# Kernel tuning notes

Hardware: AMD Instinct MI355X
Metric: run time of the kernel (lower is better)

## Reference

```python
import jax, jax.numpy as jnp
import numpy as np

NEG_SLOPE = 0.2  # PyG GATConv default negative_slope
EPS = 1e-16


def gat_conv(x, src, dst, num_nodes, W, a_src, a_dst, bias, heads, out_c, concat):
    """PyG-style GATConv (eval mode, self-loops already appended).
    x: [N, F_in]; src/dst: [E] (edge j->i with src=j, dst=i).
    W: [F_in, heads*out_c]; a_src/a_dst: [heads, out_c]; bias: [heads*out_c] or [out_c].
    """
    xw = (x @ W).reshape(num_nodes, heads, out_c)          # [N, H, C]
    alpha_src = jnp.sum(xw * a_src, axis=-1)               # [N, H]
    alpha_dst = jnp.sum(xw * a_dst, axis=-1)               # [N, H]
    e = jax.nn.leaky_relu(alpha_src[src] + alpha_dst[dst], NEG_SLOPE)  # [E, H]
    # numerically stable segment softmax over edges grouped by destination node
    m = jax.ops.segment_max(e, dst, num_segments=num_nodes)            # [N, H]
    e = jnp.exp(e - m[dst])
    denom = jax.ops.segment_sum(e, dst, num_segments=num_nodes)        # [N, H]
    alpha = e / (denom[dst] + EPS)                                     # [E, H]
    # weighted scatter-sum aggregation of source messages
    out = jax.ops.segment_sum(xw[src] * alpha[:, :, None], dst, num_segments=num_nodes)  # [N, H, C]
    if concat:
        out = out.reshape(num_nodes, heads * out_c)
    else:
        out = out.mean(axis=1)
    return out + bias


def setup_inputs() -> dict:
    key = jax.random.key(0)
    ks = jax.random.split(key, 12)
    N, E = 50000, 800000
    F_in, Hid, H1, Out = 512, 32, 8, 64

    def xavier(k, shape, gain=1.414):
        fan_in, fan_out = shape[0], shape[-1] if len(shape) == 2 else int(np.prod(shape[1:]))
        a = gain * np.sqrt(6.0 / (fan_in + fan_out))
        return jax.random.uniform(k, shape, jnp.float32, -a, a)

    x = jax.random.normal(ks[0], (N, F_in), jnp.float32)
    edge_index = jax.random.randint(ks[1], (2, E), 0, N, jnp.int64)

    W1 = xavier(ks[2], (F_in, H1 * Hid))
    a_src1 = xavier(ks[3], (H1, Hid))
    a_dst1 = xavier(ks[4], (H1, Hid))
    b1 = jnp.zeros((H1 * Hid,), jnp.float32)

    W2 = xavier(ks[5], (H1 * Hid, Out))
    a_src2 = xavier(ks[6], (1, Out))
    a_dst2 = xavier(ks[7], (1, Out))
    b2 = jnp.zeros((Out,), jnp.float32)

    return {"x": x, "edge_index": edge_index,
            "W1": W1, "a_src1": a_src1, "a_dst1": a_dst1, "b1": b1,
            "W2": W2, "a_src2": a_src2, "a_dst2": a_dst2, "b2": b2}


def reference(x, edge_index, W1, a_src1, a_dst1, b1, W2, a_src2, a_dst2, b2):
    N = x.shape[0]
    # add self-loops (PyG GATConv default add_self_loops=True)
    loop = jnp.arange(N, dtype=edge_index.dtype)
    src = jnp.concatenate([edge_index[0], loop])
    dst = jnp.concatenate([edge_index[1], loop])

    # eval mode: all dropouts are identity
    h = gat_conv(x, src, dst, N, W1, a_src1, a_dst1, b1, heads=8, out_c=32, concat=True)
    h = jax.nn.elu(h)
    h = gat_conv(h, src, dst, N, W2, a_src2, a_dst2, b2, heads=1, out_c=64, concat=False)
    return jax.nn.log_softmax(h, axis=1)
```

## Files before the change

### kernel.cpp

```cpp
#include <hip/hip_runtime.h>
#include <hip/hip_bf16.h>


typedef __attribute__((ext_vector_type(8)))  __bf16          bf16x8;
typedef __attribute__((ext_vector_type(8)))  unsigned short  ushort8;
typedef __attribute__((ext_vector_type(16))) float           f32x16;
typedef __attribute__((ext_vector_type(2)))  float           f32x2;

#define NEG_SLOPE 0.2f
#define EPS_GAT 1e-16f

static __device__ __forceinline__ float lrelu(float x) {
    return x > 0.0f ? x : NEG_SLOPE * x;
}
static __device__ __forceinline__ unsigned short f2bf(float f) {
    unsigned u = __float_as_uint(f);
    return (unsigned short)((u + 0x7fffu + ((u >> 16) & 1u)) >> 16);
}
static __device__ __forceinline__ float bf2f(unsigned short v) {
    return __uint_as_float(((unsigned)v) << 16);
}
static __device__ __forceinline__ unsigned encf(float x) {
    unsigned u = __float_as_uint(x);
    return (u >> 31) ? ~u : (u | 0x80000000u);
}
static __device__ __forceinline__ float decf(unsigned e) {
    unsigned u = (e >> 31) ? (e & 0x7fffffffu) : ~e;
    return __uint_as_float(u);
}

__global__ void k_hist_w(const void* __restrict__ eix, int* __restrict__ counts,
                         int E, int EB,
                         const float* __restrict__ W1, const float* __restrict__ W2,
                         unsigned short* __restrict__ w1t, unsigned short* __restrict__ w2t) {
    int b = blockIdx.x;
    if (b < EB) {
        int i = b * 256 + threadIdx.x;
        unsigned w = ((const unsigned*)eix)[2 * min(i, E - 1) + 1];
        bool is64 = (__syncthreads_or((int)(w != 0u)) == 0);
        if (i < E) {
            int d = is64 ? (int)((const long long*)eix)[E + i]
                         : ((const int*)eix)[E + i];
            atomicAdd(&counts[d], 1);
        }
    } else {
        int t = (b - EB) * 256 + threadIdx.x;
        if (t < 512 * 256) {
            int k = t >> 8, m = t & 255;
            w1t[m * 512 + k] = f2bf(W1[t]);
        } else {
            int u = t - 512 * 256;
            if (u < 256 * 64) {
                int k = u >> 6, m = u & 63;
                w2t[m * 256 + k] = f2bf(W2[u]);
            }
        }
    }
}

__global__ void k_scan1(const int* __restrict__ counts, int* __restrict__ rowp,
                        int* __restrict__ bsum, int N) {
    __shared__ int s[256];
    int t = threadIdx.x, i = blockIdx.x * 256 + t;
    int v = (i < N) ? counts[i] : 0;
    s[t] = v;
    __syncthreads();
    for (int off = 1; off < 256; off <<= 1) {
        int u = (t >= off) ? s[t - off] : 0;
        __syncthreads();
        s[t] += u;
        __syncthreads();
    }
    if (i < N) rowp[i] = s[t] - v;
    if (t == 255) bsum[blockIdx.x] = s[255];
}

__global__ void k_scan2(const int* __restrict__ bsum, int* __restrict__ boff,
                        int* __restrict__ rowp_last, int NB) {
    __shared__ int s[256];
    int t = threadIdx.x;
    int v = (t < NB) ? bsum[t] : 0;
    s[t] = v;
    __syncthreads();
    for (int off = 1; off < 256; off <<= 1) {
        int u = (t >= off) ? s[t - off] : 0;
        __syncthreads();
        s[t] += u;
        __syncthreads();
    }
    if (t < NB) boff[t] = s[t] - v;
    if (t == 255) *rowp_last = s[255];
}

__global__ void k_scan3(int* __restrict__ rowp, int* __restrict__ cursor,
                        const int* __restrict__ boff, int N) {
    int i = blockIdx.x * 256 + threadIdx.x;
    if (i < N) {
        int r = rowp[i] + boff[blockIdx.x];
        rowp[i] = r;
        cursor[i] = r;
    }
}

__global__ void k_fill(const void* __restrict__ eix, int* __restrict__ cursor,
                       int* __restrict__ ssrc, int E) {
    int i = blockIdx.x * 256 + threadIdx.x;
    unsigned w = ((const unsigned*)eix)[2 * min(i, E - 1) + 1];
    bool is64 = (__syncthreads_or((int)(w != 0u)) == 0);
    if (i >= E) return;
    int s, d;
    if (is64) {
        s = (int)((const long long*)eix)[i];
        d = (int)((const long long*)eix)[E + i];
    } else {
        s = ((const int*)eix)[i];
        d = ((const int*)eix)[E + i];
    }
    int pos = atomicAdd(&cursor[d], 1);
    ssrc[pos] = s;
}

template <int BM, int BN, int NT, bool AF32, bool OUTBF>
__global__ __launch_bounds__(NT) void k_gemm(const void* __restrict__ Ain,
                                             const unsigned short* __restrict__ Bt,
                                             void* __restrict__ Cout, int Nrows, int K) {
    constexpr int LD = 40;
    constexpr int AIT = BM * 4 / NT;
    constexpr int BIT = BN * 4 / NT;
    __shared__ __align__(16) unsigned short As[BM * LD];
    __shared__ __align__(16) unsigned short Bs[BN * LD];
    const int tid = threadIdx.x;
    const int blockRow = blockIdx.x * BM;
    const int wave = tid >> 6, lane = tid & 63;
    constexpr int WR = BM / 64;
    const int wr = wave % WR, wc = wave / WR;
    const int m = lane & 31;
    const int ksel = (lane >> 5) * 8;

    f32x16 acc00{}, acc01{}, acc10{}, acc11{};

    float4  af0[AIT], af1[AIT];
    ushort8 ab[AIT];
    ushort8 bb[BIT];

    auto loadA = [&](int kt) {
        #pragma unroll
        for (int i = 0; i < AIT; ++i) {
            int idx = tid + i * NT;
            int r = idx >> 2, kc = (idx & 3) * 8;
            int grow = blockRow + r;
            if constexpr (AF32) {
                const float* A = (const float*)Ain;
                if (grow < Nrows) {
                    const float* ap = A + (size_t)grow * K + kt + kc;
                    af0[i] = *(const float4*)ap;
                    af1[i] = *(const float4*)(ap + 4);
                } else {
                    af0[i] = make_float4(0.f, 0.f, 0.f, 0.f);
                    af1[i] = make_float4(0.f, 0.f, 0.f, 0.f);
                }
            } else {
                const unsigned short* A = (const unsigned short*)Ain;
                ushort8 o{};
                if (grow < Nrows) o = *(const ushort8*)(A + (size_t)grow * K + kt + kc);
                ab[i] = o;
            }
        }
    };
    auto loadB = [&](int kt) {
        #pragma unroll
        for (int i = 0; i < BIT; ++i) {
            int idx = tid + i * NT;
            int r = idx >> 2, kc = (idx & 3) * 8;
            bb[i] = *(const ushort8*)(Bt + (size_t)r * K + kt + kc);
        }
    };
    auto writeAB = [&]() {
        #pragma unroll
        for (int i = 0; i < AIT; ++i) {
            int idx = tid + i * NT;
            int r = idx >> 2, kc = (idx & 3) * 8;
            if constexpr (AF32) {
                union { ushort8 u; __hip_bfloat162 h[4]; } cv;
                cv.h[0] = __float22bfloat162_rn(make_float2(af0[i].x, af0[i].y));
                cv.h[1] = __float22bfloat162_rn(make_float2(af0[i].z, af0[i].w));
                cv.h[2] = __float22bfloat162_rn(make_float2(af1[i].x, af1[i].y));
                cv.h[3] = __float22bfloat162_rn(make_float2(af1[i].z, af1[i].w));
                *(ushort8*)&As[r * LD + kc] = cv.u;
            } else {
                *(ushort8*)&As[r * LD + kc] = ab[i];
            }
        }
        #pragma unroll
        for (int i = 0; i < BIT; ++i) {
            int idx = tid + i * NT;
            int r = idx >> 2, kc = (idx & 3) * 8;
            *(ushort8*)&Bs[r * LD + kc] = bb[i];
        }
    };

    loadA(0);
    loadB(0);
    for (int kt = 0; kt < K; kt += 32) {
        writeAB();
        __syncthreads();
        if (kt + 32 < K) {
            loadA(kt + 32);
            loadB(kt + 32);
        }
        #pragma unroll
        for (int kk = 0; kk < 32; kk += 16) {
            bf16x8 a0 = *(const bf16x8*)&As[(wr * 64 +      m) * LD + kk + ksel];
            bf16x8 a1 = *(const bf16x8*)&As[(wr * 64 + 32 + m) * LD + kk + ksel];
            bf16x8 b0 = *(const bf16x8*)&Bs[(wc * 64 +      m) * LD + kk + ksel];
            bf16x8 b1 = *(const bf16x8*)&Bs[(wc * 64 + 32 + m) * LD + kk + ksel];
            acc00 = __builtin_amdgcn_mfma_f32_32x32x16_bf16(a0, b0, acc00, 0, 0, 0);
            acc01 = __builtin_amdgcn_mfma_f32_32x32x16_bf16(a0, b1, acc01, 0, 0, 0);
            acc10 = __builtin_amdgcn_mfma_f32_32x32x16_bf16(a1, b0, acc10, 0, 0, 0);
            acc11 = __builtin_amdgcn_mfma_f32_32x32x16_bf16(a1, b1, acc11, 0, 0, 0);
        }
        __syncthreads();
    }

    const int dcol = wc * 64 + (lane & 31);
    const int dquad = 4 * (lane >> 5);
    auto store_tile = [&](const f32x16& a, int rt, int ct) {
        #pragma unroll
        for (int r = 0; r < 16; ++r) {
            int row = blockRow + wr * 64 + rt * 32 + (r & 3) + 8 * (r >> 2) + dquad;
            if (row < Nrows) {
                size_t off = (size_t)row * BN + dcol + ct * 32;
                if constexpr (OUTBF) ((unsigned short*)Cout)[off] = f2bf(a[r]);
                else                 ((float*)Cout)[off] = a[r];
            }
        }
    };
    store_tile(acc00, 0, 0); store_tile(acc01, 0, 1);
    store_tile(acc10, 1, 0); store_tile(acc11, 1, 1);
}

__global__ void k_alpha(const unsigned short* __restrict__ xw, const float* __restrict__ a_s,
                        const float* __restrict__ a_d, float* __restrict__ os,
                        float* __restrict__ od, unsigned* __restrict__ Menc,
                        int NH, int H, int C) {
    __shared__ float red[256];
    int t = blockIdx.x * 256 + threadIdx.x;
    float s = -1e30f, d = 0.f;
    if (t < NH) {
        int n = t / H, h = t - n * H;
        const unsigned short* row = xw + (size_t)n * H * C + h * C;
        s = 0.f;
        for (int c = 0; c < C; c += 8) {
            ushort8 v = *(const ushort8*)(row + c);
            #pragma unroll
            for (int q = 0; q < 8; ++q) {
                float f = bf2f(v[q]);
                s += f * a_s[h * C + c + q];
                d += f * a_d[h * C + c + q];
            }
        }
        os[t] = s; od[t] = d;
    }
    red[threadIdx.x] = s;
    __syncthreads();
    for (int off = 128; off >= H; off >>= 1) {
        if (threadIdx.x < off) red[threadIdx.x] = fmaxf(red[threadIdx.x], red[threadIdx.x + off]);
        __syncthreads();
    }
    if ((int)threadIdx.x < H) atomicMax(&Menc[threadIdx.x], encf(red[threadIdx.x]));
}

__global__ __launch_bounds__(256, 6) void k_agg_l1(
        const unsigned short* __restrict__ xw1, const float* __restrict__ asrc,
        const float* __restrict__ adst, const unsigned* __restrict__ Menc,
        const float* __restrict__ b1, const int* __restrict__ rp,
        const int* __restrict__ ssrc, unsigned short* __restrict__ hbf, int N) {
    int wid = (blockIdx.x * 256 + threadIdx.x) >> 6;
    if (wid >= N) return;
    const int lane = threadIdx.x & 63;
    const int g  = lane >> 4;
    const int q  = lane & 15;
    const int f0 = q * 16;
    const int h  = q >> 1;
    const int ih = wid * 8 + h;
    const float ad = adst[ih];
    const float m  = lrelu(decf(Menc[h]) + ad);
    f32x2 acc[8];
    float s;
    {
        float w = (g == 0) ? __expf(lrelu(asrc[ih] + ad) - m) : 0.0f;
        const unsigned short* pr = xw1 + (size_t)wid * 256 + f0;
        ushort8 lo = *(const ushort8*)pr;
        ushort8 hi = *(const ushort8*)(pr + 8);
        s = w;
        const unsigned* dl = (const unsigned*)&lo;
        const unsigned* dh = (const unsigned*)&hi;
        #pragma unroll
        for (int p = 0; p < 4; ++p) {
            acc[p].x     = w * __uint_as_float(dl[p] << 16);
            acc[p].y     = w * __uint_as_float(dl[p] & 0xffff0000u);
            acc[4 + p].x = w * __uint_as_float(dh[p] << 16);
            acc[4 + p].y = w * __uint_as_float(dh[p] & 0xffff0000u);
        }
    }
    const int e0 = rp[wid], e1 = rp[wid + 1];
    if (e0 < e1) {
        const int NQ = (e1 - e0 + 3) >> 2;

        auto LDJ = [&](int base, int& j, bool& v) {
            v = base + g < e1;
            j = ssrc[min(base + g, e1 - 1)];
        };
        auto LDD = [&](int j, float& as, ushort8& lo, ushort8& hi) {
            as = asrc[j * 8 + h];
            const unsigned short* p = xw1 + ((size_t)j << 8) + f0;
            lo = *(const ushort8*)p;
            hi = *(const ushort8*)(p + 8);
        };
        auto CONS = [&](bool v, float as, const ushort8& lo, const ushort8& hi) {
            float w = v ? __expf(lrelu(as + ad) - m) : 0.0f;
            s += w;
            f32x2 wp; wp.x = w; wp.y = w;
            const unsigned* dl = (const unsigned*)&lo;
            const unsigned* dh = (const unsigned*)&hi;
            #pragma unroll
            for (int p = 0; p < 4; ++p) {
                f32x2 x;
                x.x = __uint_as_float(dl[p] << 16);
                x.y = __uint_as_float(dl[p] & 0xffff0000u);
                asm("v_pk_fma_f32 %0, %1, %2, %3"
                    : "=v"(acc[p]) : "v"(x), "v"(wp), "v"(acc[p]));
            }
            #pragma unroll
            for (int p = 0; p < 4; ++p) {
                f32x2 x;
                x.x = __uint_as_float(dh[p] << 16);
                x.y = __uint_as_float(dh[p] & 0xffff0000u);
                asm("v_pk_fma_f32 %0, %1, %2, %3"
                    : "=v"(acc[4 + p]) : "v"(x), "v"(wp), "v"(acc[4 + p]));
            }
        };

        int j0, j1, j2, j3; bool v0, v1, v2, v3;
        float as0, as1; ushort8 lo0, hi0, lo1, hi1;
        LDJ(e0,      j0, v0);
        LDJ(e0 + 4,  j1, v1);
        LDD(j0, as0, lo0, hi0);
        LDJ(e0 + 8,  j2, v2);
        LDD(j1, as1, lo1, hi1);
        LDJ(e0 + 12, j3, v3);

        #pragma unroll 2
        for (int k = 0; k < NQ - 2; ++k) {
            int jN; bool vN;
            LDJ(e0 + 4 * k + 16, jN, vN);
            float as2; ushort8 lo2, hi2;
            LDD(j2, as2, lo2, hi2);
            CONS(v0, as0, lo0, hi0);
            v0 = v1; as0 = as1; lo0 = lo1; hi0 = hi1;
            v1 = v2; as1 = as2; lo1 = lo2; hi1 = hi2;
            v2 = v3; j2 = j3;
            v3 = vN; j3 = jN;
        }
        CONS(v0, as0, lo0, hi0);
        if (NQ >= 2) CONS(v1, as1, lo1, hi1);
    }
    s += __shfl_xor(s, 16, 64);
    s += __shfl_xor(s, 32, 64);
    #pragma unroll
    for (int p = 0; p < 8; ++p) {
        acc[p].x += __shfl_xor(acc[p].x, 16, 64);
        acc[p].x += __shfl_xor(acc[p].x, 32, 64);
        acc[p].y += __shfl_xor(acc[p].y, 16, 64);
        acc[p].y += __shfl_xor(acc[p].y, 32, 64);
    }
    float inv = 1.0f / (s + EPS_GAT);
    f32x2 p0 = (g & 2) ? ((g & 1) ? acc[6] : acc[4]) : ((g & 1) ? acc[2] : acc[0]);
    f32x2 p1 = (g & 2) ? ((g & 1) ? acc[7] : acc[5]) : ((g & 1) ? acc[3] : acc[1]);
    int fw = f0 + g * 4;
    float vv[4] = { p0.x, p0.y, p1.x, p1.y };
    ushort4 o;
    #pragma unroll
    for (int i = 0; i < 4; ++i) {
        float v = vv[i] * inv + b1[fw + i];
        v = v > 0.f ? v : expm1f(v);
        ((unsigned short*)&o)[i] = f2bf(v);
    }
    *(ushort4*)(hbf + (size_t)wid * 256 + fw) = o;
}

__global__ __launch_bounds__(256, 6) void k_agg_l2(
        const unsigned short* __restrict__ xw2, const float* __restrict__ asrc,
        const float* __restrict__ adst, const unsigned* __restrict__ Menc,
        const float* __restrict__ b2, const int* __restrict__ rp,
        const int* __restrict__ ssrc, float* __restrict__ out, int N) {
    int wid = (blockIdx.x * 256 + threadIdx.x) >> 6;
    if (wid >= N) return;
    const int lane = threadIdx.x & 63;
    const int g  = lane >> 3;
    const int q  = lane & 7;
    const int f0 = q * 8;
    const float ad = adst[wid];
    const float m = lrelu(decf(Menc[0]) + ad);
    f32x2 acc[4];
    float s;
    {
        float w = (g == 0) ? __expf(lrelu(asrc[wid] + ad) - m) : 0.0f;
        ushort8 xv = *(const ushort8*)(xw2 + (size_t)wid * 64 + f0);
        s = w;
        const unsigned* dx = (const unsigned*)&xv;
        #pragma unroll
        for (int p = 0; p < 4; ++p) {
            acc[p].x = w * __uint_as_float(dx[p] << 16);
            acc[p].y = w * __uint_as_float(dx[p] & 0xffff0000u);
        }
    }
    const int e0 = rp[wid], e1 = rp[wid + 1];
    if (e0 < e1) {
        const int NQ = (e1 - e0 + 7) >> 3;

        auto LDJ = [&](int base, int& j, bool& v) {
            v = base + g < e1;
            j = ssrc[min(base + g, e1 - 1)];
        };
        auto LDD = [&](int j, float& as, ushort8& xv) {
            as = asrc[j];
            xv = *(const ushort8*)(xw2 + ((size_t)j << 6) + f0);
        };
        auto CONS = [&](bool v, float as, const ushort8& xv) {
            float w = v ? __expf(lrelu(as + ad) - m) : 0.0f;
            s += w;
            f32x2 wp; wp.x = w; wp.y = w;
            const unsigned* dx = (const unsigned*)&xv;
            #pragma unroll
            for (int p = 0; p < 4; ++p) {
                f32x2 x;
                x.x = __uint_as_float(dx[p] << 16);
                x.y = __uint_as_float(dx[p] & 0xffff0000u);
                asm("v_pk_fma_f32 %0, %1, %2, %3"
                    : "=v"(acc[p]) : "v"(x), "v"(wp), "v"(acc[p]));
            }
        };

        int j0, j1, j2, j3; bool v0, v1, v2, v3;
        float as0, as1; ushort8 xv0, xv1;
        LDJ(e0,      j0, v0);
        LDJ(e0 + 8,  j1, v1);
        LDD(j0, as0, xv0);
        LDJ(e0 + 16, j2, v2);
        LDD(j1, as1, xv1);
        LDJ(e0 + 24, j3, v3);

        #pragma unroll 2
        for (int k = 0; k < NQ - 2; ++k) {
            int jN; bool vN;
            LDJ(e0 + 8 * k + 32, jN, vN);
            float as2; ushort8 xv2;
            LDD(j2, as2, xv2);
            CONS(v0, as0, xv0);
            v0 = v1; as0 = as1; xv0 = xv1;
            v1 = v2; as1 = as2; xv1 = xv2;
            v2 = v3; j2 = j3;
            v3 = vN; j3 = jN;
        }
        CONS(v0, as0, xv0);
        if (NQ >= 2) CONS(v1, as1, xv1);
    }
    s += __shfl_xor(s, 8, 64);
    s += __shfl_xor(s, 16, 64);
    s += __shfl_xor(s, 32, 64);
    #pragma unroll
    for (int p = 0; p < 4; ++p) {
        acc[p].x += __shfl_xor(acc[p].x, 8, 64);
        acc[p].x += __shfl_xor(acc[p].x, 16, 64);
        acc[p].x += __shfl_xor(acc[p].x, 32, 64);
        acc[p].y += __shfl_xor(acc[p].y, 8, 64);
        acc[p].y += __shfl_xor(acc[p].y, 16, 64);
        acc[p].y += __shfl_xor(acc[p].y, 32, 64);
    }
    float inv = 1.0f / (s + EPS_GAT);
    float val[8];
    float mx = -1e30f;
    #pragma unroll
    for (int i = 0; i < 8; ++i) {
        float a = (i & 1) ? acc[i >> 1].y : acc[i >> 1].x;
        val[i] = a * inv + b2[f0 + i];
        mx = fmaxf(mx, val[i]);
    }
    #pragma unroll
    for (int off = 4; off > 0; off >>= 1) mx = fmaxf(mx, __shfl_xor(mx, off, 64));
    float sm = 0.f;
    #pragma unroll
    for (int i = 0; i < 8; ++i) sm += __expf(val[i] - mx);
    #pragma unroll
    for (int off = 4; off > 0; off >>= 1) sm += __shfl_xor(sm, off, 64);
    float lse = mx + logf(sm);
    if (g == 0) {
        float4 o0 = make_float4(val[0] - lse, val[1] - lse, val[2] - lse, val[3] - lse);
        float4 o1 = make_float4(val[4] - lse, val[5] - lse, val[6] - lse, val[7] - lse);
        *(float4*)(out + (size_t)wid * 64 + f0)     = o0;
        *(float4*)(out + (size_t)wid * 64 + f0 + 4) = o1;
    }
}

static inline int cdiv(int a, int b) { return (a + b - 1) / b; }

extern "C" void kernel_launch(void* const* d_in, const int* in_sizes, int n_in,
                              void* d_out, int out_size, void* d_ws, size_t ws_size,
                              hipStream_t stream) {
    const float* x   = (const float*)d_in[0];
    const void*  eix = d_in[1];
    const float* W1  = (const float*)d_in[2];
    const float* as1 = (const float*)d_in[3];
    const float* ad1 = (const float*)d_in[4];
    const float* b1  = (const float*)d_in[5];
    const float* W2  = (const float*)d_in[6];
    const float* as2 = (const float*)d_in[7];
    const float* ad2 = (const float*)d_in[8];
    const float* b2  = (const float*)d_in[9];
    float* out = (float*)d_out;

    const int N = in_sizes[0] / 512;
    const int E = in_sizes[1] / 2;
    const int EB = cdiv(E, 256);
    const int WB = cdiv(512 * 256 + 256 * 64, 256);
    const int NB = cdiv(N, 256);
    const int NB1 = cdiv(N * 8, 256);
    const int NB2 = cdiv(N, 256);
    (void)n_in; (void)out_size; (void)ws_size;

    char* base = (char*)d_ws;
    size_t o = 0;
    auto alloc = [&](size_t bytes) -> char* {
        o = (o + 255) & ~(size_t)255;
        char* p = base + o;
        o += bytes;
        return p;
    };
    unsigned short* xw1b  = (unsigned short*)alloc((size_t)N * 256 * 2);
    unsigned short* hbf   = (unsigned short*)alloc((size_t)N * 256 * 2);
    unsigned short* xw2b  = (unsigned short*)alloc((size_t)N * 64 * 2);
    float*          asrc1 = (float*)alloc((size_t)N * 8 * 4);
    float*          adst1 = (float*)alloc((size_t)N * 8 * 4);
    float*          asrc2 = (float*)alloc((size_t)N * 4);
    float*          adst2 = (float*)alloc((size_t)N * 4);
    size_t zero_begin = (o + 255) & ~(size_t)255;
    unsigned*       Menc  = (unsigned*)alloc(16 * 4);
    int*            counts= (int*)alloc((size_t)N * 4);
    size_t zero_end = o;
    int*            cursor= (int*)alloc((size_t)N * 4);
    int*            rowp  = (int*)alloc((size_t)(N + 1) * 4);
    int*            bsum  = (int*)alloc(256 * 4);
    int*            boff  = (int*)alloc(256 * 4);
    unsigned short* w1t   = (unsigned short*)alloc(512 * 256 * 2);
    unsigned short* w2t   = (unsigned short*)alloc(256 * 64 * 2);
    int*            ssrc  = (int*)alloc((size_t)E * 4);

    hipMemsetAsync(base + zero_begin, 0, zero_end - zero_begin, stream);

    k_hist_w<<<EB + WB, 256, 0, stream>>>(eix, counts, E, EB, W1, W2, w1t, w2t);
    k_scan1<<<NB, 256, 0, stream>>>(counts, rowp, bsum, N);
    k_scan2<<<1, 256, 0, stream>>>(bsum, boff, rowp + N, NB);
    k_scan3<<<NB, 256, 0, stream>>>(rowp, cursor, boff, N);
    k_fill<<<EB, 256, 0, stream>>>(eix, cursor, ssrc, E);

    k_gemm<128, 256, 512, true, true><<<cdiv(N, 128), 512, 0, stream>>>(x, w1t, xw1b, N, 512);
    k_alpha<<<NB1, 256, 0, stream>>>(xw1b, as1, ad1, asrc1, adst1, Menc, N * 8, 8, 32);
    k_agg_l1<<<cdiv(N * 64, 256), 256, 0, stream>>>(xw1b, asrc1, adst1, Menc, b1,
                                                    rowp, ssrc, hbf, N);
    k_gemm<256, 64, 256, false, true><<<cdiv(N, 256), 256, 0, stream>>>(hbf, w2t, xw2b, N, 256);
    k_alpha<<<NB2, 256, 0, stream>>>(xw2b, as2, ad2, asrc2, adst2, Menc + 8, N, 1, 64);
    k_agg_l2<<<cdiv(N * 64, 256), 256, 0, stream>>>(xw2b, asrc2, adst2, Menc + 8, b2,
                                                    rowp, ssrc, out, N);
}
```

Measured before the change: 416.7 us.

## Store layer-1 features head-major and aggregate one head per block

The first GEMM now writes its output head-major ([H][N][32]), and the alpha kernel reads and writes in that layout. The layer-1 aggregation kernel is restructured so each block handles a single head for four nodes. Each wave processes 16 edges at a time, and each lane gathers a 16-byte slice of one head's row instead of full 512-byte rows. The aim is better cache locality, since each head's 3.2MB slice fits in cache when blocks are grouped by head, at the cost of more edge-index loads and a shallower prefetch pipeline than the previous four-stage software pipeline.

After: 582.0 us. +39.7%, slower.

```diff
diff --git a/kernel.cpp b/kernel.cpp
--- a/kernel.cpp
+++ b/kernel.cpp
@@ -120,7 +120,7 @@
     ssrc[pos] = s;
 }
 
-template <int BM, int BN, int NT, bool AF32, bool OUTBF>
+template <int BM, int BN, int NT, bool AF32, bool OUTBF, bool OUTHM>
 __global__ __launch_bounds__(NT) void k_gemm(const void* __restrict__ Ain,
                                              const unsigned short* __restrict__ Bt,
                                              void* __restrict__ Cout, int Nrows, int K) {
@@ -229,7 +229,12 @@
         for (int r = 0; r < 16; ++r) {
             int row = blockRow + wr * 64 + rt * 32 + (r & 3) + 8 * (r >> 2) + dquad;
             if (row < Nrows) {
-                size_t off = (size_t)row * BN + dcol + ct * 32;
+                int col = dcol + ct * 32;
+                size_t off;
+                if constexpr (OUTHM)
+                    off = ((size_t)(col >> 5) * Nrows + row) * 32 + (col & 31);
+                else
+                    off = (size_t)row * BN + col;
                 if constexpr (OUTBF) ((unsigned short*)Cout)[off] = f2bf(a[r]);
                 else                 ((float*)Cout)[off] = a[r];
             }
@@ -242,13 +247,13 @@
 __global__ void k_alpha(const unsigned short* __restrict__ xw, const float* __restrict__ a_s,
                         const float* __restrict__ a_d, float* __restrict__ os,
                         float* __restrict__ od, unsigned* __restrict__ Menc,
-                        int NH, int H, int C) {
+                        int NH, int H, int C, int Nn) {
     __shared__ float red[256];
     int t = blockIdx.x * 256 + threadIdx.x;
     float s = -1e30f, d = 0.f;
     if (t < NH) {
         int n = t / H, h = t - n * H;
-        const unsigned short* row = xw + (size_t)n * H * C + h * C;
+        const unsigned short* row = xw + ((size_t)h * Nn + n) * C;
         s = 0.f;
         for (int c = 0; c < C; c += 8) {
             ushort8 v = *(const ushort8*)(row + c);
@@ -259,7 +264,8 @@
                 d += f * a_d[h * C + c + q];
             }
         }
-        os[t] = s; od[t] = d;
+        size_t oi = (size_t)h * Nn + n;
+        os[oi] = s; od[oi] = d;
     }
     red[threadIdx.x] = s;
     __syncthreads();
@@ -271,122 +277,86 @@
 }
 
 __global__ __launch_bounds__(256, 6) void k_agg_l1(
-        const unsigned short* __restrict__ xw1, const float* __restrict__ asrc,
-        const float* __restrict__ adst, const unsigned* __restrict__ Menc,
+        const unsigned short* __restrict__ xwh,
+        const float* __restrict__ asrc,
+        const float* __restrict__ adst,
+        const unsigned* __restrict__ Menc,
         const float* __restrict__ b1, const int* __restrict__ rp,
         const int* __restrict__ ssrc, unsigned short* __restrict__ hbf, int N) {
-    int wid = (blockIdx.x * 256 + threadIdx.x) >> 6;
-    if (wid >= N) return;
+    const int h  = blockIdx.x & 7;
+    const int n  = (blockIdx.x >> 3) * 4 + (threadIdx.x >> 6);
+    if (n >= N) return;
     const int lane = threadIdx.x & 63;
-    const int g  = lane >> 4;
-    const int q  = lane & 15;
-    const int f0 = q * 16;
-    const int h  = q >> 1;
-    const int ih = wid * 8 + h;
-    const float ad = adst[ih];
+    const int g  = lane & 15;
+    const int c8 = (lane >> 4) * 8;
+    const size_t hN = (size_t)h * N;
+    const float ad = adst[hN + n];
     const float m  = lrelu(decf(Menc[h]) + ad);
-    f32x2 acc[8];
+    f32x2 acc[4];
     float s;
     {
-        float w = (g == 0) ? __expf(lrelu(asrc[ih] + ad) - m) : 0.0f;
-        const unsigned short* pr = xw1 + (size_t)wid * 256 + f0;
-        ushort8 lo = *(const ushort8*)pr;
-        ushort8 hi = *(const ushort8*)(pr + 8);
+        float w = (g == 0) ? __expf(lrelu(asrc[hN + n] + ad) - m) : 0.0f;
+        ushort8 xv = *(const ushort8*)(xwh + (hN + n) * 32 + c8);
         s = w;
-        const unsigned* dl = (const unsigned*)&lo;
-        const unsigned* dh = (const unsigned*)&hi;
+        const unsigned* dx = (const unsigned*)&xv;
         #pragma unroll
         for (int p = 0; p < 4; ++p) {
-            acc[p].x     = w * __uint_as_float(dl[p] << 16);
-            acc[p].y     = w * __uint_as_float(dl[p] & 0xffff0000u);
-            acc[4 + p].x = w * __uint_as_float(dh[p] << 16);
-            acc[4 + p].y = w * __uint_as_float(dh[p] & 0xffff0000u);
-        }
-    }
-    const int e0 = rp[wid], e1 = rp[wid + 1];
+            acc[p].x = w * __uint_as_float(dx[p] << 16);
+            acc[p].y = w * __uint_as_float(dx[p] & 0xffff0000u);
+        }
+    }
+    const int e0 = rp[n], e1 = rp[n + 1];
     if (e0 < e1) {
-        const int NQ = (e1 - e0 + 3) >> 2;
-
-        auto LDJ = [&](int base, int& j, bool& v) {
-            v = base + g < e1;
-            j = ssrc[min(base + g, e1 - 1)];
-        };
-        auto LDD = [&](int j, float& as, ushort8& lo, ushort8& hi) {
-            as = asrc[j * 8 + h];
-            const unsigned short* p = xw1 + ((size_t)j << 8) + f0;
-            lo = *(const ushort8*)p;
-            hi = *(const ushort8*)(p + 8);
-        };
-        auto CONS = [&](bool v, float as, const ushort8& lo, const ushort8& hi) {
-            float w = v ? __expf(lrelu(as + ad) - m) : 0.0f;
+        int k = e0;
+        bool vA = k + g < e1;
+        int jA = ssrc[min(k + g, e1 - 1)];
+        while (true) {
+            int kn = k + 16;
+            bool hasN = kn < e1;
+            bool vB = false; int jB = 0;
+            if (hasN) { vB = kn + g < e1; jB = ssrc[min(kn + g, e1 - 1)]; }
+            float as = asrc[hN + jA];
+            ushort8 xv = *(const ushort8*)(xwh + (hN + jA) * 32 + c8);
+            float w = vA ? __expf(lrelu(as + ad) - m) : 0.0f;
             s += w;
             f32x2 wp; wp.x = w; wp.y = w;
-            const unsigned* dl = (const unsigned*)&lo;
-            const unsigned* dh = (const unsigned*)&hi;
+            const unsigned* dx = (const unsigned*)&xv;
             #pragma unroll
             for (int p = 0; p < 4; ++p) {
                 f32x2 x;
-                x.x = __uint_as_float(dl[p] << 16);
-                x.y = __uint_as_float(dl[p] & 0xffff0000u);
+                x.x = __uint_as_float(dx[p] << 16);
+                x.y = __uint_as_float(dx[p] & 0xffff0000u);
                 asm("v_pk_fma_f32 %0, %1, %2, %3"
                     : "=v"(acc[p]) : "v"(x), "v"(wp), "v"(acc[p]));
             }
-            #pragma unroll
-            for (int p = 0; p < 4; ++p) {
-                f32x2 x;
-                x.x = __uint_as_float(dh[p] << 16);
-                x.y = __uint_as_float(dh[p] & 0xffff0000u);
-                asm("v_pk_fma_f32 %0, %1, %2, %3"
-                    : "=v"(acc[4 + p]) : "v"(x), "v"(wp), "v"(acc[4 + p]));
-            }
-        };
-
-        int j0, j1, j2, j3; bool v0, v1, v2, v3;
-        float as0, as1; ushort8 lo0, hi0, lo1, hi1;
-        LDJ(e0,      j0, v0);
-        LDJ(e0 + 4,  j1, v1);
-        LDD(j0, as0, lo0, hi0);
-        LDJ(e0 + 8,  j2, v2);
-        LDD(j1, as1, lo1, hi1);
-        LDJ(e0 + 12, j3, v3);
-
-        #pragma unroll 2
-        for (int k = 0; k < NQ - 2; ++k) {
-            int jN; bool vN;
-            LDJ(e0 + 4 * k + 16, jN, vN);
-            float as2; ushort8 lo2, hi2;
-            LDD(j2, as2, lo2, hi2);
-            CONS(v0, as0, lo0, hi0);
-            v0 = v1; as0 = as1; lo0 = lo1; hi0 = hi1;
-            v1 = v2; as1 = as2; lo1 = lo2; hi1 = hi2;
-            v2 = v3; j2 = j3;
-            v3 = vN; j3 = jN;
-        }
-        CONS(v0, as0, lo0, hi0);
-        if (NQ >= 2) CONS(v1, as1, lo1, hi1);
-    }
-    s += __shfl_xor(s, 16, 64);
-    s += __shfl_xor(s, 32, 64);
+            if (!hasN) break;
+            vA = vB; jA = jB; k = kn;
+        }
+    }
     #pragma unroll
-    for (int p = 0; p < 8; ++p) {
-        acc[p].x += __shfl_xor(acc[p].x, 16, 64);
-        acc[p].x += __shfl_xor(acc[p].x, 32, 64);
-        acc[p].y += __shfl_xor(acc[p].y, 16, 64);
-        acc[p].y += __shfl_xor(acc[p].y, 32, 64);
-    }
-    float inv = 1.0f / (s + EPS_GAT);
-    f32x2 p0 = (g & 2) ? ((g & 1) ? acc[6] : acc[4]) : ((g & 1) ? acc[2] : acc[0]);
-    f32x2 p1 = (g & 2) ? ((g & 1) ? acc[7] : acc[5]) : ((g & 1) ? acc[3] : acc[1]);
-    int fw = f0 + g * 4;
-    float vv[4] = { p0.x, p0.y, p1.x, p1.y };
-    ushort4 o;
-    #pragma unroll
-    for (int i = 0; i < 4; ++i) {
-        float v = vv[i] * inv + b1[fw + i];
-        v = v > 0.f ? v : expm1f(v);
-        ((unsigned short*)&o)[i] = f2bf(v);
-    }
-    *(ushort4*)(hbf + (size_t)wid * 256 + fw) = o;
+    for (int off = 1; off <= 8; off <<= 1) {
+        s += __shfl_xor(s, off, 64);
+        #pragma unroll
+        for (int p = 0; p < 4; ++p) {
+            acc[p].x += __shfl_xor(acc[p].x, off, 64);
+            acc[p].y += __shfl_xor(acc[p].y, off, 64);
+        }
+    }
+    if (g == 0) {
+        float inv = 1.0f / (s + EPS_GAT);
+        int fb = h * 32 + c8;
+        ushort8 o;
+        #pragma unroll
+        for (int p = 0; p < 4; ++p) {
+            float v0 = acc[p].x * inv + b1[fb + 2 * p];
+            float v1 = acc[p].y * inv + b1[fb + 2 * p + 1];
+            v0 = v0 > 0.f ? v0 : expm1f(v0);
+            v1 = v1 > 0.f ? v1 : expm1f(v1);
+            ((unsigned short*)&o)[2 * p]     = f2bf(v0);
+            ((unsigned short*)&o)[2 * p + 1] = f2bf(v1);
+        }
+        *(ushort8*)(hbf + (size_t)n * 256 + fb) = o;
+    }
 }
 
 __global__ __launch_bounds__(256, 6) void k_agg_l2(
@@ -564,12 +534,12 @@
     k_scan3<<<NB, 256, 0, stream>>>(rowp, cursor, boff, N);
     k_fill<<<EB, 256, 0, stream>>>(eix, cursor, ssrc, E);
 
-    k_gemm<128, 256, 512, true, true><<<cdiv(N, 128), 512, 0, stream>>>(x, w1t, xw1b, N, 512);
-    k_alpha<<<NB1, 256, 0, stream>>>(xw1b, as1, ad1, asrc1, adst1, Menc, N * 8, 8, 32);
-    k_agg_l1<<<cdiv(N * 64, 256), 256, 0, stream>>>(xw1b, asrc1, adst1, Menc, b1,
-                                                    rowp, ssrc, hbf, N);
-    k_gemm<256, 64, 256, false, true><<<cdiv(N, 256), 256, 0, stream>>>(hbf, w2t, xw2b, N, 256);
-    k_alpha<<<NB2, 256, 0, stream>>>(xw2b, as2, ad2, asrc2, adst2, Menc + 8, N, 1, 64);
+    k_gemm<128, 256, 512, true, true, true><<<cdiv(N, 128), 512, 0, stream>>>(x, w1t, xw1b, N, 512);
+    k_alpha<<<NB1, 256, 0, stream>>>(xw1b, as1, ad1, asrc1, adst1, Menc, N * 8, 8, 32, N);
+    k_agg_l1<<<cdiv(N, 4) * 8, 256, 0, stream>>>(xw1b, asrc1, adst1, Menc, b1,
+                                                 rowp, ssrc, hbf, N);
+    k_gemm<256, 64, 256, false, true, false><<<cdiv(N, 256), 256, 0, stream>>>(hbf, w2t, xw2b, N, 256);
+    k_alpha<<<NB2, 256, 0, stream>>>(xw2b, as2, ad2, asrc2, adst2, Menc + 8, N, 1, 64, N);
     k_agg_l2<<<cdiv(N * 64, 256), 256, 0, stream>>>(xw2b, asrc2, adst2, Menc + 8, b2,
                                                     rowp, ssrc, out, N);
 }
```
